# Kernel tuning notes

Hardware: AMD Instinct MI355X
Metric: run time of the kernel (lower is better)

## Reference

```python
import jax, jax.numpy as jnp
import numpy as np
from functools import partial

# Straight-through sign (Binarize): sign forward, identity gradient
@jax.custom_vjp
def ste_sign(x):
    return jnp.sign(x)

def _ste_fwd(x):
    return jnp.sign(x), None

def _ste_bwd(_, g):
    return (g,)

ste_sign.defvjp(_ste_fwd, _ste_bwd)


def conv2d(x, w):
    # x: [N,C,H,W], w: [O,I,kh,kw], VALID conv, stride 1
    return jax.lax.conv_general_dilated(
        x, w, window_strides=(1, 1), padding='VALID',
        dimension_numbers=('NCHW', 'OIHW', 'NCHW'))


def maxpool2x2(x):
    return jax.lax.reduce_window(
        x, -jnp.inf, jax.lax.max, (1, 1, 2, 2), (1, 1, 2, 2), 'VALID')


def setup_inputs() -> dict:
    key = jax.random.key(0)
    ks = jax.random.split(key, 32)
    d = {}
    d['x'] = jax.random.normal(ks[0], (128, 3, 32, 32), dtype=jnp.float32)
    wshapes = [(128, 3, 3, 3), (128, 128, 3, 3), (256, 128, 3, 3),
               (256, 256, 3, 3), (512, 256, 3, 3), (512, 512, 3, 3),
               (10, 512, 4, 4)]
    for i, s in enumerate(wshapes):
        d[f'w{i+1}'] = jax.random.normal(ks[1 + i], s, dtype=jnp.float32) * 0.05
    bn_ch = [128, 128, 256, 256, 512, 512, 10]
    for i, c in enumerate(bn_ch):
        d[f'bn{i+1}_s'] = jax.random.uniform(ks[10 + 2 * i], (c,), dtype=jnp.float32,
                                             minval=0.5, maxval=1.5)
        d[f'bn{i+1}_t'] = jax.random.normal(ks[11 + 2 * i], (c,), dtype=jnp.float32) * 0.1
    return d


def _forward(x, w1, w2, w3, w4, w5, w6, w7,
             bn1_s, bn1_t, bn2_s, bn2_t, bn3_s, bn3_t, bn4_s, bn4_t,
             bn5_s, bn5_t, bn6_s, bn6_t, bn7_s, bn7_t):
    def block(h, w, s, t, pool, binarize_in):
        if binarize_in:
            h = ste_sign(h)            # binarize activations (in_ch != 3)
        h = jnp.pad(h, ((0, 0), (0, 0), (1, 1), (1, 1)))  # F.pad value=0
        h = conv2d(h, ste_sign(w))      # binarized weights
        if pool:
            h = maxpool2x2(h)
        h = h * s[None, :, None, None] + t[None, :, None, None]  # eval BN
        return jnp.clip(h, -1.0, 1.0)   # Hardtanh

    h = block(x, w1, bn1_s, bn1_t, pool=False, binarize_in=False)  # 32x32x128
    h = block(h, w2, bn2_s, bn2_t, pool=True,  binarize_in=True)   # 16x16x128
    h = block(h, w3, bn3_s, bn3_t, pool=False, binarize_in=True)   # 16x16x256
    h = block(h, w4, bn4_s, bn4_t, pool=True,  binarize_in=True)   # 8x8x256
    h = block(h, w5, bn5_s, bn5_t, pool=False, binarize_in=True)   # 8x8x512
    h = block(h, w6, bn6_s, bn6_t, pool=True,  binarize_in=True)   # 4x4x512
    # conv7: binarize input + weights, 4x4 kernel, no padding -> [N,10,1,1]
    h = conv2d(ste_sign(h), ste_sign(w7))
    h = h.reshape(-1, 10)
    h = h * bn7_s + bn7_t               # eval BatchNorm1d(10)
    return jax.nn.log_softmax(h, axis=1)


def reference(x, w1, w2, w3, w4, w5, w6, w7,
              bn1_s, bn1_t, bn2_s, bn2_t, bn3_s, bn3_t, bn4_s, bn4_t,
              bn5_s, bn5_t, bn6_s, bn6_t, bn7_s, bn7_t):
    return _forward(x, w1, w2, w3, w4, w5, w6, w7,
                    bn1_s, bn1_t, bn2_s, bn2_t, bn3_s, bn3_t, bn4_s, bn4_t,
                    bn5_s, bn5_t, bn6_s, bn6_t, bn7_s, bn7_t)
```

## Files before the change

kernel.cpp:

```cpp
#include <hip/hip_runtime.h>
#include <cstdint>
#include <math.h>

#define NB 128

__global__ void pack_all_kernel(
    const float* __restrict__ w1,
    const float* __restrict__ w2, const float* __restrict__ w3,
    const float* __restrict__ w4, const float* __restrict__ w5,
    const float* __restrict__ w6, const float* __restrict__ w7,
    const float* __restrict__ s2, const float* __restrict__ t2,
    const float* __restrict__ s3, const float* __restrict__ t3,
    const float* __restrict__ s4, const float* __restrict__ t4,
    const float* __restrict__ s5, const float* __restrict__ t5,
    const float* __restrict__ s6, const float* __restrict__ t6,
    float* __restrict__ wsf,
    uint32_t* __restrict__ wp2, uint32_t* __restrict__ wp3,
    uint32_t* __restrict__ wp4, uint32_t* __restrict__ wp5,
    uint32_t* __restrict__ wp6, uint32_t* __restrict__ wp7,
    int* __restrict__ thr) {
  int i = blockIdx.x * 256 + threadIdx.x;
  if (i >= 150528) return;
  if (i >= 147072) {
    int j = i - 147072;
    wsf[j] = (w1[j] >= 0.0f) ? 1.0f : -1.0f;
    return;
  }
  if (i >= 145408) {
    int j = i - 145408;
    const float *bsp, *btp; int idx;
    if (j < 128)       { bsp = s2; btp = t2; idx = j; }
    else if (j < 384)  { bsp = s3; btp = t3; idx = j - 128; }
    else if (j < 640)  { bsp = s4; btp = t4; idx = j - 384; }
    else if (j < 1152) { bsp = s5; btp = t5; idx = j - 640; }
    else               { bsp = s6; btp = t6; idx = j - 1152; }
    const double s = (double)bsp[idx], t = (double)btp[idx];
    int d0 = (int)floor(-t / s);
    int th = d0 + 4;
    for (int d = d0 - 3; d <= d0 + 4; ++d)
      if ((double)d * s + t >= 0.0) { th = d; break; }
    thr[j] = th;
    return;
  }
  const float* w; uint32_t* wp; int C, KHW; bool nl = true;
  if (i < 4608)        { w = w2; wp = wp2; C = 128; KHW = 9; }
  else if (i < 13824)  { i -= 4608;   w = w3; wp = wp3; C = 128; KHW = 9; }
  else if (i < 32256)  { i -= 13824;  w = w4; wp = wp4; C = 256; KHW = 9; }
  else if (i < 69120)  { i -= 32256;  w = w5; wp = wp5; C = 256; KHW = 9; }
  else if (i < 142848) { i -= 69120;  w = w6; wp = wp6; C = 512; KHW = 9; }
  else                 { i -= 142848; w = w7; wp = wp7; C = 512; KHW = 16; nl = false; }
  int Cw = C >> 5;
  int cw = i % Cw;
  int rest = i / Cw;
  int t = rest % KHW;
  int o = rest / KHW;
  uint32_t word = 0;
  for (int b = 0; b < 32; ++b)
    word |= ((w[(o * C + cw * 32 + b) * KHW + t] >= 0.0f) ? 1u : 0u) << b;
  if (nl) {
    const int ocg = o >> 6, lane = o & 63, pass = cw >> 2, cwi = cw & 3;
    wp[(((ocg * (Cw >> 2) + pass) * 9 + t) * 64 + lane) * 4 + cwi] = word;
  } else {
    wp[(o * KHW + t) * Cw + cw] = word;
  }
}

__device__ __forceinline__ int v_zero() {
  return __builtin_amdgcn_ds_bpermute(0, 0);
}

__device__ __forceinline__ void popc_acc(int& acc, uint32_t x) {
  asm("v_bcnt_u32_b32 %0, %1, %0" : "+v"(acc) : "v"(x));
}

__global__ __launch_bounds__(256, 2) void conv1_kernel(
    const float* __restrict__ x, const float* __restrict__ wsf,
    const float* __restrict__ bs, const float* __restrict__ bt,
    uint32_t* __restrict__ out) {
  const int tid = blockIdx.x * 256 + threadIdx.x;
  const int og = blockIdx.y;
  const int px = tid & 31, py = (tid >> 5) & 31, n = tid >> 10;

  float xv[27];
#pragma unroll
  for (int ic = 0; ic < 3; ++ic)
#pragma unroll
    for (int kh = 0; kh < 3; ++kh) {
      const int yy = py + kh - 1;
      const int yc = min(max(yy, 0), 31);
      const float* row = x + ((n * 3 + ic) * 32 + yc) * 32;
#pragma unroll
      for (int kw = 0; kw < 3; ++kw) {
        const int xx = px + kw - 1;
        const int xc = min(max(xx, 0), 31);
        const float v = row[xc];
        const bool ok = ((unsigned)yy < 32u) && ((unsigned)xx < 32u);
        xv[ic * 9 + kh * 3 + kw] = ok ? v : 0.0f;
      }
    }

  uint32_t wout = 0;
  const float* wog = wsf + og * 32 * 27;
#pragma unroll
  for (int o4 = 0; o4 < 8; ++o4) {
    float a0 = 0.f, a1 = 0.f, a2 = 0.f, a3 = 0.f;
#pragma unroll
    for (int t = 0; t < 27; ++t) {
      a0 = fmaf(xv[t], wog[(o4 * 4 + 0) * 27 + t], a0);
      a1 = fmaf(xv[t], wog[(o4 * 4 + 1) * 27 + t], a1);
      a2 = fmaf(xv[t], wog[(o4 * 4 + 2) * 27 + t], a2);
      a3 = fmaf(xv[t], wog[(o4 * 4 + 3) * 27 + t], a3);
    }
    float aa[4] = {a0, a1, a2, a3};
#pragma unroll
    for (int j = 0; j < 4; ++j) {
      const int ob = o4 * 4 + j;
      const int oc = og * 32 + ob;
      const float s = bs[oc], t0 = bt[oc];
      const float v = fmaf(aa[j], s, t0);
      bool pos = v >= 0.0f;
      if (fabsf(v) < 1e-3f * s) {
        double ad = 0.0;
        for (int t = 0; t < 27; ++t)
          ad += (double)wog[ob * 27 + t] * (double)xv[t];
        pos = (ad * (double)s + (double)t0) >= 0.0;
      }
      wout |= (pos ? 1u : 0u) << ob;
    }
  }
  out[tid * 4 + og] = wout;
}

template <int CW, int CWP, int H, int W, int PC, int R, bool POOL, int WPB>
__global__ __launch_bounds__(64 * WPB, 5) void bconv_kernel(
    const uint32_t* __restrict__ act, const uint32_t* __restrict__ wpk,
    const int* __restrict__ thrp,
    uint32_t* __restrict__ out, int OCW) {
  static_assert(CW % CWP == 0 && CWP == 4, "");
  const int lane = threadIdx.x & 63;
  const int ocg = blockIdx.y;
  const int zero = v_zero();
  const int cpr = W / PC;
  const int wid = __builtin_amdgcn_readfirstlane((int)(threadIdx.x >> 6));
  const int g = blockIdx.x * WPB + wid;
  const int cg = g % cpr;
  const int rg = (g / cpr) % (H / R);
  const int n  = g / (cpr * (H / R));
  const int y0 = rg * R, x0 = cg * PC;

  const int thr = thrp[ocg * 64 + lane];

  int acc[R * PC];
#pragma unroll
  for (int p = 0; p < R * PC; ++p) acc[p] = 0;

#pragma unroll 1
  for (int pass = 0; pass < CW / CWP; ++pass) {
    uint32_t wreg[9 * CWP];
    {
      const uint32_t* wbase =
          wpk + (((ocg * (CW / CWP) + pass) * 9) * 64 + lane) * 4;
#pragma unroll
      for (int t = 0; t < 9; ++t)
        *(uint4*)&wreg[t * 4] = *(const uint4*)(wbase + t * 256);
    }

#pragma unroll
    for (int ry = -1; ry <= R; ++ry) {
      const int y = y0 + ry;
      if (y < 0 || y >= H) continue;
      const uint32_t* rowp = act + zero + (((size_t)n * H + y) * W + x0) * CW + pass * CWP;
      uint32_t buf[(PC + 2) * CWP];
#pragma unroll
      for (int cc = -1; cc <= PC; ++cc) {
        const int x = x0 + cc;
        if (x < 0 || x >= W) continue;
#pragma unroll
        for (int q = 0; q < CWP / 4; ++q)
          *(uint4*)&buf[(cc + 1) * CWP + q * 4] =
              *(const uint4*)(rowp + cc * CW + q * 4);
      }
#pragma unroll
      for (int cc = -1; cc <= PC; ++cc) {
        const int x = x0 + cc;
        if (x < 0 || x >= W) continue;
#pragma unroll
        for (int r = 0; r < R; ++r) {
          const int kh = ry - r + 1;
          if (kh < 0 || kh > 2) continue;
#pragma unroll
          for (int kw = 0; kw < 3; ++kw) {
            const int pxo = cc - kw + 1;
            if (pxo < 0 || pxo >= PC) continue;
#pragma unroll
            for (int cw = 0; cw < CWP; ++cw)
              popc_acc(acc[r * PC + pxo],
                       buf[(cc + 1) * CWP + cw] ^ wreg[(kh * 3 + kw) * CWP + cw]);
          }
        }
      }
    }
  }

  if (!POOL) {
    uint64_t bal[R * PC];
#pragma unroll
    for (int r = 0; r < R; ++r)
#pragma unroll
      for (int pxo = 0; pxo < PC; ++pxo) {
        const int y = y0 + r, x = x0 + pxo;
        const int nv32 =
            32 * CW * (3 - (y == 0) - (y == H - 1)) * (3 - (x == 0) - (x == W - 1));
        bal[r * PC + pxo] = __ballot(acc[r * PC + pxo] <= ((nv32 - thr) >> 1));
      }
    if (lane == 0) {
#pragma unroll
      for (int r = 0; r < R; ++r)
#pragma unroll
        for (int pxo = 0; pxo < PC; ++pxo)
          *(uint64_t*)(out + ((n * H + (y0 + r)) * W + (x0 + pxo)) * OCW + ocg * 2) =
              bal[r * PC + pxo];
    }
  } else {
    static_assert(!POOL || R == 2, "pool needs row pairs");
    uint64_t pooled[PC / 2];
#pragma unroll
    for (int c2 = 0; c2 < PC / 2; ++c2) pooled[c2] = 0;
#pragma unroll
    for (int r = 0; r < R; ++r)
#pragma unroll
      for (int pxo = 0; pxo < PC; ++pxo) {
        const int y = y0 + r, x = x0 + pxo;
        const int nv32 =
            32 * CW * (3 - (y == 0) - (y == H - 1)) * (3 - (x == 0) - (x == W - 1));
        pooled[pxo >> 1] |= __ballot(acc[r * PC + pxo] <= ((nv32 - thr) >> 1));
      }
    if (lane == 0) {
#pragma unroll
      for (int c2 = 0; c2 < PC / 2; ++c2) {
        const int yo = y0 >> 1, xo = (x0 >> 1) + c2;
        *(uint64_t*)(out + ((n * (H / 2) + yo) * (W / 2) + xo) * OCW + ocg * 2) =
            pooled[c2];
      }
    }
  }
}

__global__ __launch_bounds__(64) void conv7_kernel(
    const uint32_t* __restrict__ act, const uint32_t* __restrict__ wp,
    const float* __restrict__ bs, const float* __restrict__ bt,
    float* __restrict__ out) {
  int n = blockIdx.x;
  int lane = threadIdx.x;
  const uint32_t* a = act + n * 256;
  __shared__ double logits[10];
  for (int o = 0; o < 10; ++o) {
    int acc = 0;
    for (int w = lane; w < 256; w += 64) acc += __popc(a[w] ^ wp[o * 256 + w]);
    for (int off = 32; off > 0; off >>= 1) acc += __shfl_down(acc, off, 64);
    if (lane == 0) {
      double dotd = (double)(8192 - 2 * acc);
      logits[o] = dotd * (double)bs[o] + (double)bt[o];
    }
  }
  __syncthreads();
  if (lane == 0) {
    double m = logits[0];
    for (int o = 1; o < 10; ++o) m = fmax(m, logits[o]);
    double s = 0.0;
    for (int o = 0; o < 10; ++o) s += exp(logits[o] - m);
    double lse = log(s);
    for (int o = 0; o < 10; ++o) out[n * 10 + o] = (float)(logits[o] - m - lse);
  }
}

extern "C" void kernel_launch(void* const* d_in, const int* in_sizes, int n_in,
                              void* d_out, int out_size, void* d_ws, size_t ws_size,
                              hipStream_t stream) {
  const float* x  = (const float*)d_in[0];
  const float* w1 = (const float*)d_in[1];
  const float* w2 = (const float*)d_in[2];
  const float* w3 = (const float*)d_in[3];
  const float* w4 = (const float*)d_in[4];
  const float* w5 = (const float*)d_in[5];
  const float* w6 = (const float*)d_in[6];
  const float* w7 = (const float*)d_in[7];
  const float* s1 = (const float*)d_in[8];  const float* t1 = (const float*)d_in[9];
  const float* s2 = (const float*)d_in[10]; const float* t2 = (const float*)d_in[11];
  const float* s3 = (const float*)d_in[12]; const float* t3 = (const float*)d_in[13];
  const float* s4 = (const float*)d_in[14]; const float* t4 = (const float*)d_in[15];
  const float* s5 = (const float*)d_in[16]; const float* t5 = (const float*)d_in[17];
  const float* s6 = (const float*)d_in[18]; const float* t6 = (const float*)d_in[19];
  const float* s7 = (const float*)d_in[20]; const float* t7 = (const float*)d_in[21];
  float* out = (float*)d_out;

  uint32_t* ws = (uint32_t*)d_ws;
  uint32_t* A   = ws;
  uint32_t* B   = ws + 524288;
  uint32_t* wp2 = ws + 1048576;
  uint32_t* wp3 = wp2 + 4608;
  uint32_t* wp4 = wp3 + 9216;
  uint32_t* wp5 = wp4 + 18432;
  uint32_t* wp6 = wp5 + 36864;
  uint32_t* wp7 = wp6 + 73728;
  float* wsf    = (float*)(wp7 + 2560);
  int* thr      = (int*)(wsf + 3456);

  pack_all_kernel<<<dim3(588), dim3(256), 0, stream>>>(
      w1, w2, w3, w4, w5, w6, w7,
      s2, t2, s3, t3, s4, t4, s5, t5, s6, t6,
      wsf, wp2, wp3, wp4, wp5, wp6, wp7, thr);

  conv1_kernel<<<dim3(512, 4), dim3(256), 0, stream>>>(x, wsf, s1, t1, A);

  bconv_kernel<4, 4, 32, 32, 4, 2, true, 4>
      <<<dim3(4096, 2), dim3(256), 0, stream>>>(A, wp2, thr + 0, B, 4);

  bconv_kernel<4, 4, 16, 16, 4, 2, false, 4>
      <<<dim3(1024, 4), dim3(256), 0, stream>>>(B, wp3, thr + 128, A, 8);

  bconv_kernel<8, 4, 16, 16, 4, 2, true, 4>
      <<<dim3(1024, 4), dim3(256), 0, stream>>>(A, wp4, thr + 384, B, 8);

  bconv_kernel<8, 4, 8, 8, 4, 2, false, 4>
      <<<dim3(256, 8), dim3(256), 0, stream>>>(B, wp5, thr + 640, A, 16);

  bconv_kernel<16, 4, 8, 8, 4, 2, true, 4>
      <<<dim3(256, 8), dim3(256), 0, stream>>>(A, wp6, thr + 1152, B, 16);

  conv7_kernel<<<dim3(128), dim3(64), 0, stream>>>(B, wp7, s7, t7, out);
}
```

Before: 293.0 us.

## Stage binarized activation rows in LDS shared by all waves of a block

Each block now cooperatively copies the activation rows its waves need (the row span plus a one-row halo) into shared memory, then synchronizes. The per-wave inner loop reads from LDS instead of global memory. This removes the ds_bpermute zero trick that was used to force vector loads. The aim is to cut repeated global/L2 traffic for overlapping halo rows across waves. In exchange it adds LDS usage that may lower occupancy, plus a block barrier, and it assumes all waves in a block share the same image.

```diff
diff --git a/kernel.cpp b/kernel.cpp
--- a/kernel.cpp
+++ b/kernel.cpp
@@ -65,10 +65,6 @@
   }
 }
 
-__device__ __forceinline__ int v_zero() {
-  return __builtin_amdgcn_ds_bpermute(0, 0);
-}
-
 __device__ __forceinline__ void popc_acc(int& acc, uint32_t x) {
   asm("v_bcnt_u32_b32 %0, %1, %0" : "+v"(acc) : "v"(x));
 }
@@ -137,15 +133,36 @@
     const int* __restrict__ thrp,
     uint32_t* __restrict__ out, int OCW) {
   static_assert(CW % CWP == 0 && CWP == 4, "");
+  constexpr int CPR = W / PC;
+  constexpr int SPANRG = (CPR >= WPB) ? 1 : (WPB / CPR);
+  constexpr int S = SPANRG * R + 2;
+  constexpr int RW = W * CW;
+  __shared__ uint32_t alds[S * RW];
+
   const int lane = threadIdx.x & 63;
   const int ocg = blockIdx.y;
-  const int zero = v_zero();
-  const int cpr = W / PC;
+  const int gb = blockIdx.x * WPB;
+  const int nB  = gb / (CPR * (H / R));
+  const int rg0 = (gb / CPR) % (H / R);
+  const int ymin = rg0 * R - 1;
+
+  {
+    const uint32_t* actn = act + (size_t)nB * H * RW;
+    for (int idx = threadIdx.x; idx < S * RW / 4; idx += 64 * WPB) {
+      const int s = idx / (RW / 4);
+      const int c4 = idx - s * (RW / 4);
+      const int y = ymin + s;
+      if ((unsigned)y < (unsigned)H)
+        *(uint4*)&alds[s * RW + c4 * 4] =
+            *(const uint4*)(actn + (size_t)y * RW + c4 * 4);
+    }
+  }
+  __syncthreads();
+
   const int wid = __builtin_amdgcn_readfirstlane((int)(threadIdx.x >> 6));
-  const int g = blockIdx.x * WPB + wid;
-  const int cg = g % cpr;
-  const int rg = (g / cpr) % (H / R);
-  const int n  = g / (cpr * (H / R));
+  const int g = gb + wid;
+  const int cg = g % CPR;
+  const int rg = (g / CPR) % (H / R);
   const int y0 = rg * R, x0 = cg * PC;
 
   const int thr = thrp[ocg * 64 + lane];
@@ -169,7 +186,7 @@
     for (int ry = -1; ry <= R; ++ry) {
       const int y = y0 + ry;
       if (y < 0 || y >= H) continue;
-      const uint32_t* rowp = act + zero + (((size_t)n * H + y) * W + x0) * CW + pass * CWP;
+      const uint32_t* lrow = alds + (y - ymin) * RW + x0 * CW + pass * CWP;
       uint32_t buf[(PC + 2) * CWP];
 #pragma unroll
       for (int cc = -1; cc <= PC; ++cc) {
@@ -178,7 +195,7 @@
 #pragma unroll
         for (int q = 0; q < CWP / 4; ++q)
           *(uint4*)&buf[(cc + 1) * CWP + q * 4] =
-              *(const uint4*)(rowp + cc * CW + q * 4);
+              *(const uint4*)(lrow + cc * CW + q * 4);
       }
 #pragma unroll
       for (int cc = -1; cc <= PC; ++cc) {
@@ -218,7 +235,7 @@
       for (int r = 0; r < R; ++r)
 #pragma unroll
         for (int pxo = 0; pxo < PC; ++pxo)
-          *(uint64_t*)(out + ((n * H + (y0 + r)) * W + (x0 + pxo)) * OCW + ocg * 2) =
+          *(uint64_t*)(out + ((nB * H + (y0 + r)) * W + (x0 + pxo)) * OCW + ocg * 2) =
               bal[r * PC + pxo];
     }
   } else {
@@ -239,7 +256,7 @@
 #pragma unroll
       for (int c2 = 0; c2 < PC / 2; ++c2) {
         const int yo = y0 >> 1, xo = (x0 >> 1) + c2;
-        *(uint64_t*)(out + ((n * (H / 2) + yo) * (W / 2) + xo) * OCW + ocg * 2) =
+        *(uint64_t*)(out + ((nB * (H / 2) + yo) * (W / 2) + xo) * OCW + ocg * 2) =
             pooled[c2];
       }
     }
```

Result: no change. 296.0 us (+1.0%).
